# Kernel optimization log

Hardware: AMD Instinct MI355X
Metric: run time of the kernel (lower is better)

The kernel has to match this reference:

```python
import jax, jax.numpy as jnp
import numpy as np

B, H, W = 8, 448, 448
HID, EMB, OUT = 1024, 1024, 4096
P = 12544
hgrid = wgrid = H // 14  # 32


def layernorm2d(x, wgt, bias, eps=1e-6):
    # channel-wise LN over dim 1 per spatial location, as in LayerNorm2d
    u = x.mean(1, keepdims=True)
    s = ((x - u) ** 2).mean(1, keepdims=True)
    x = (x - u) / jnp.sqrt(s + eps)
    return wgt[None, :, None, None] * x + bias[None, :, None, None]


def conv2d(x, wk, b, stride):
    y = jax.lax.conv_general_dilated(x, wk, (stride, stride), 'VALID',
                                     dimension_numbers=('NCHW', 'OIHW', 'NCHW'))
    return y + b[None, :, None, None]


def grid_sample_bilinear(feat, grid):
    # feat [B,C,h,w]; grid [B,P,2] (x,y) in [-1,1]; align_corners=False, zeros padding
    Bc, C, Hh, Ww = feat.shape
    gx = (grid[..., 0] + 1.0) * 0.5 * Ww - 0.5
    gy = (grid[..., 1] + 1.0) * 0.5 * Hh - 0.5
    x0 = jnp.floor(gx); y0 = jnp.floor(gy)
    x1 = x0 + 1.0; y1 = y0 + 1.0
    wx1 = gx - x0; wx0 = 1.0 - wx1
    wy1 = gy - y0; wy0 = 1.0 - wy1
    flat = feat.reshape(Bc, C, Hh * Ww)

    def gather(ix, iy):
        valid = (ix >= 0) & (ix < Ww) & (iy >= 0) & (iy < Hh)
        ixc = jnp.clip(ix, 0, Ww - 1).astype(jnp.int32)
        iyc = jnp.clip(iy, 0, Hh - 1).astype(jnp.int32)
        idx = iyc * Ww + ixc  # [B,P]
        g = jnp.take_along_axis(flat, idx[:, None, :], axis=2)  # [B,C,P]
        return g * valid[:, None, :].astype(g.dtype)

    return (gather(x0, y0) * (wx0 * wy0)[:, None, :]
            + gather(x1, y0) * (wx1 * wy0)[:, None, :]
            + gather(x0, y1) * (wx0 * wy1)[:, None, :]
            + gather(x1, y1) * (wx1 * wy1)[:, None, :])


def forward(images, masks, image_features, point_coords, valid_mask,
            c1w, c1b, ln1w, ln1b, c2w, c2b, ln2w, ln2b, c3w, c3b, up_w, up_b):
    x = jnp.concatenate([images, masks], axis=1)  # [B,4,H,W]
    x = conv2d(x, c1w, c1b, 7)
    x = jax.nn.gelu(layernorm2d(x, ln1w, ln1b), approximate=False)
    x = conv2d(x, c2w, c2b, 2)
    x = jax.nn.gelu(layernorm2d(x, ln2w, ln2b), approximate=False)
    x = conv2d(x, c3w, c3b, 1)  # [B,EMB,h,w]
    feat = image_features.reshape(B, hgrid, wgrid, EMB).transpose(0, 3, 1, 2)
    x = x + feat
    # point_sample: coords in [0,1], mapped to [-1,1]
    sf = grid_sample_bilinear(x, 2.0 * point_coords - 1.0)  # [B,EMB,P]
    sf = sf.transpose(0, 2, 1)  # [B,P,EMB]
    vm = valid_mask.astype(sf.dtype)
    pooled = (sf * vm[:, :, None]).sum(1) / vm.sum(1)[:, None]
    pooled = jnp.nan_to_num(pooled)
    out = pooled @ up_w.T + up_b  # [B,OUT]
    return out  # single feature level: stack([out]).mean(0) == out


def setup_inputs() -> dict:
    key = jax.random.key(0)
    ks = jax.random.split(key, 12)
    rng = np.random.default_rng(0)

    masks_np = np.zeros((B, 1, H, W), np.float32)
    coords = np.full((B, P, 2), -1.0, np.float32)
    valid = np.zeros((B, P), bool)
    for b in range(B):
        y0r = int(rng.integers(0, H // 2)); x0r = int(rng.integers(0, W // 2))
        hh = int(rng.integers(H // 4, H // 2)); ww = int(rng.integers(W // 4, W // 2))
        masks_np[b, 0, y0r:y0r + hh, x0r:x0r + ww] = 1.0
        ys, xs = np.nonzero(masks_np[b, 0])
        n = len(ys)
        sel = np.sort(rng.choice(n, size=min(P, n), replace=False))
        k = len(sel)
        coords[b, :k, 0] = xs[sel] / W  # x normalized (flip of (y,x))
        coords[b, :k, 1] = ys[sel] / H  # y normalized
        valid[b, :k] = True

    s = 0.02
    return {
        'images': jax.random.normal(ks[0], (B, 3, H, W), jnp.float32),
        'masks': jnp.asarray(masks_np),
        'image_features': jax.random.normal(ks[1], (B, hgrid * wgrid, EMB), jnp.float32),
        'point_coords': jnp.asarray(coords),
        'valid_mask': jnp.asarray(valid),
        'c1w': jax.random.normal(ks[2], (HID // 4, 4, 7, 7), jnp.float32) * s,
        'c1b': jnp.zeros((HID // 4,), jnp.float32),
        'ln1w': jnp.ones((HID // 4,), jnp.float32),
        'ln1b': jnp.zeros((HID // 4,), jnp.float32),
        'c2w': jax.random.normal(ks[3], (HID, HID // 4, 2, 2), jnp.float32) * s,
        'c2b': jnp.zeros((HID,), jnp.float32),
        'ln2w': jnp.ones((HID,), jnp.float32),
        'ln2b': jnp.zeros((HID,), jnp.float32),
        'c3w': jax.random.normal(ks[4], (EMB, HID, 1, 1), jnp.float32) * s,
        'c3b': jnp.zeros((EMB,), jnp.float32),
        'up_w': jax.random.normal(ks[5], (OUT, EMB), jnp.float32) * s,
        'up_b': jnp.zeros((OUT,), jnp.float32),
    }


def reference(images, masks, image_features, point_coords, valid_mask,
              c1w, c1b, ln1w, ln1b, c2w, c2b, ln2w, ln2b, c3w, c3b, up_w, up_b):
    return forward(images, masks, image_features, point_coords, valid_mask,
                   c1w, c1b, ln1w, ln1b, c2w, c2b, ln2w, ln2b, c3w, c3b, up_w, up_b)
```

## Files before the change

kernel.cpp:

```cpp
#include <hip/hip_runtime.h>
#include <stdint.h>

#define NB 8
#define HIN 448
#define CH1 256
#define CH2 1024
#define NLOC 1024
#define M2 8192
#define M1 32768
#define K1 224
#define NPTS 12544
#define NOUT 4096
#define CAP 384
#define MC (NB * CAP)
#define M1C (MC * 4)

typedef __attribute__((ext_vector_type(8))) short bf16x8;
typedef __attribute__((ext_vector_type(4))) float f32x4;

__device__ __forceinline__ short f2bf(float f) {
  uint32_t u = __builtin_bit_cast(uint32_t, f);
  uint32_t r = (u + 0x7fffu + ((u >> 16) & 1u)) >> 16;
  return (short)r;
}
__device__ __forceinline__ float bf2f(short s) {
  return __builtin_bit_cast(float, (uint32_t)(uint16_t)s << 16);
}
__device__ __forceinline__ float gelu_f(float x) {
  return 0.5f * x * (1.0f + erff(x * 0.70710678118654752f));
}
__device__ __forceinline__ void gload_lds16(const void* g, void* l) {
  __builtin_amdgcn_global_load_lds((const __attribute__((address_space(1))) unsigned int*)g,
                                   (__attribute__((address_space(3))) unsigned int*)l, 16, 0, 0);
}

__global__ void k_prep(const float* __restrict__ c1w, const float* __restrict__ c2w,
                       short* __restrict__ c1wb, short* __restrict__ w2p,
                       float4* __restrict__ zp, int n4) {
  int i = blockIdx.x * 256 + threadIdx.x;
  if (i < n4) zp[i] = make_float4(0.f, 0.f, 0.f, 0.f);
  if (i < CH1 * K1) {
    int o = i / K1, k = i - o * K1;
    int c = k / 56, kk = k - c * 56, r = kk >> 3, cc = kk & 7;
    c1wb[i] = f2bf(cc < 7 ? c1w[((o * 4 + c) * 7 + r) * 7 + cc] : 0.0f);
  }
  if (i < CH2 * CH2) {
    int o = i >> 10, k = i & 1023;
    int pos = k >> 8, ci = k & 255;
    w2p[i] = f2bf(c2w[(size_t)(o * 256 + ci) * 4 + pos]);
  }
}

__global__ __launch_bounds__(256) void k_pts(const float* __restrict__ coords,
                                             float* __restrict__ Aw,
                                             float* __restrict__ cnt,
                                             float* __restrict__ sumAw) {
  __shared__ float lAw[NLOC];
  __shared__ int lcnt;
  __shared__ float wsum[4];
  int t = threadIdx.x;
  int b = blockIdx.x / 49;
  int blk = blockIdx.x - b * 49;
  for (int i = t; i < NLOC; i += 256) lAw[i] = 0.f;
  if (t == 0) lcnt = 0;
  __syncthreads();
  int pi = blk * 256 + t;
  float x = coords[((size_t)b * NPTS + pi) * 2];
  float y = coords[((size_t)b * NPTS + pi) * 2 + 1];
  bool valid = (x >= 0.0f);
  if (valid) {
    float gx = x * 32.0f - 0.5f, gy = y * 32.0f - 0.5f;
    float x0f = floorf(gx), y0f = floorf(gy);
    int x0 = (int)x0f, y0 = (int)y0f;
    float wx1 = gx - x0f, wx0 = 1.0f - wx1;
    float wy1 = gy - y0f, wy0 = 1.0f - wy1;
    int xs[2] = {x0, x0 + 1}, ys[2] = {y0, y0 + 1};
    float wxs[2] = {wx0, wx1}, wys[2] = {wy0, wy1};
    #pragma unroll
    for (int cy = 0; cy < 2; cy++)
      #pragma unroll
      for (int cx = 0; cx < 2; cx++) {
        int ix = xs[cx], iy = ys[cy];
        if (ix >= 0 && ix < 32 && iy >= 0 && iy < 32)
          atomicAdd(&lAw[iy * 32 + ix], wxs[cx] * wys[cy]);
      }
  }
  unsigned long long ball = __ballot(valid);
  if ((t & 63) == 0) atomicAdd(&lcnt, (int)__popcll(ball));
  __syncthreads();
  float tsum = 0.f;
  for (int i = t; i < NLOC; i += 256) {
    float v = lAw[i];
    tsum += v;
    if (v != 0.f) atomicAdd(&Aw[b * NLOC + i], v);
  }
  #pragma unroll
  for (int m = 1; m <= 32; m <<= 1) tsum += __shfl_xor(tsum, m, 64);
  if ((t & 63) == 0) wsum[t >> 6] = tsum;
  __syncthreads();
  if (t == 0) {
    float bs = wsum[0] + wsum[1] + wsum[2] + wsum[3];
    if (bs != 0.f) atomicAdd(&sumAw[b], bs);
    if (lcnt) atomicAdd(&cnt[b], (float)lcnt);
  }
}

__global__ __launch_bounds__(256) void k_compact(const float* __restrict__ Aw,
                                                 int* __restrict__ idxc,
                                                 float* __restrict__ Awc) {
  __shared__ int cnts[256], offs[256];
  int t = threadIdx.x, b = blockIdx.x;
  int base = b * 1024 + t * 4;
  float w[4];
  int c = 0;
  #pragma unroll
  for (int j = 0; j < 4; j++) { w[j] = Aw[base + j]; c += (w[j] != 0.f) ? 1 : 0; }
  cnts[t] = c;
  offs[t] = c;
  __syncthreads();
  for (int s = 1; s < 256; s <<= 1) {
    int v = (t >= s) ? offs[t - s] : 0;
    __syncthreads();
    offs[t] += v;
    __syncthreads();
  }
  int pos = b * CAP + offs[t] - cnts[t];
  int lim = (b + 1) * CAP;
  #pragma unroll
  for (int j = 0; j < 4; j++)
    if (w[j] != 0.f && pos < lim) { idxc[pos] = base + j; Awc[pos] = w[j]; pos++; }
  int total = offs[255];
  for (int i = total + t; i < CAP; i += 256) {
    idxc[b * CAP + i] = b * 1024;
    Awc[b * CAP + i] = 0.f;
  }
}

__global__ __launch_bounds__(256) void k_imc(const int* __restrict__ idxc,
                                             const float* __restrict__ images,
                                             const float* __restrict__ masks,
                                             short* __restrict__ A1c) {
  __shared__ short ct[64 * K1];
  int t = threadIdx.x;
  int i0 = blockIdx.x * 16;
  int loc = t >> 4;
  int rem = t & 15;
  int c = rem >> 2, kh = (rem >> 1) & 1, rh = rem & 1;
  int gi = idxc[i0 + loc];
  int b = gi >> 10, oy = (gi >> 5) & 31, ox = gi & 31;
  int yy = oy * 2 + kh;
  int xbase = ox * 14;
  int r0 = rh * 4, rn = rh ? 3 : 4;
  const float* plane = (c < 3)
      ? images + (size_t)(b * 3 + c) * 448 * 448
      : masks + (size_t)b * 448 * 448;
  for (int rr = 0; rr < rn; rr++) {
    int r = r0 + rr;
    const float* src = plane + (size_t)(yy * 7 + r) * 448 + xbase;
    short tmp[14];
    #pragma unroll
    for (int p = 0; p < 7; p++) {
      float2 v = *(const float2*)&src[p * 2];
      tmp[p * 2] = f2bf(v.x);
      tmp[p * 2 + 1] = f2bf(v.y);
    }
    #pragma unroll
    for (int kw = 0; kw < 2; kw++) {
      short* dst = &ct[(loc * 4 + kh * 2 + kw) * K1 + c * 56 + r * 8];
      #pragma unroll
      for (int cc = 0; cc < 7; cc++) dst[cc] = tmp[kw * 7 + cc];
      dst[7] = 0;
    }
  }
  __syncthreads();
  size_t obase = (size_t)blockIdx.x * 64 * K1;
  #pragma unroll
  for (int it = 0; it < 7; it++) {
    int p = it * 256 + t;
    *(bf16x8*)&A1c[obase + (size_t)p * 8] = *(const bf16x8*)&ct[p * 8];
  }
}

template<int KDIM, int LDC>
__global__ __launch_bounds__(256) void k_gemm64(
    const short* __restrict__ Amat, const short* __restrict__ Bmat,
    const float* __restrict__ bias, short* __restrict__ Cout) {
  __shared__ __align__(16) char Lraw[16384];
  int t = threadIdx.x, lane = t & 63, wv = t >> 6;
  int mt0 = blockIdx.x * 64;
  int nt0 = blockIdx.y * 64;
  f32x4 acc[2][2];
  #pragma unroll
  for (int i = 0; i < 2; i++)
    #pragma unroll
    for (int j = 0; j < 2; j++) acc[i][j] = (f32x4){0.f, 0.f, 0.f, 0.f};

  int srow = lane >> 2, scol = (lane & 3) * 8;
  int wm = wv >> 1, wn = wv & 1;
  int l15 = lane & 15, lg = lane >> 4;

  const short* Ap = Amat + (size_t)(mt0 + wv * 16 + srow) * KDIM;
  const short* Bp = Bmat + (size_t)(nt0 + wv * 16 + srow) * KDIM;

  auto STAGE = [&](int buf, int kt) {
    int k0 = kt * 32;
    char* As = Lraw + buf * 8192;
    char* Bs = As + 4096;
    gload_lds16(Ap + k0 + scol, As + wv * 1024);
    gload_lds16(Bp + k0 + scol, Bs + wv * 1024);
  };

  const int NT = KDIM / 32;
  STAGE(0, 0);
  __syncthreads();
  int cur = 0;
  #pragma unroll 2
  for (int kt = 0; kt < NT; kt++) {
    if (kt + 1 < NT) STAGE(cur ^ 1, kt + 1);
    const short* As = (const short*)(Lraw + cur * 8192);
    const short* Bs = As + 2048;
    bf16x8 af[2], bfr[2];
    #pragma unroll
    for (int i = 0; i < 2; i++)
      af[i] = *(const bf16x8*)&As[(wm * 32 + i * 16 + l15) * 32 + lg * 8];
    #pragma unroll
    for (int j = 0; j < 2; j++)
      bfr[j] = *(const bf16x8*)&Bs[(wn * 32 + j * 16 + l15) * 32 + lg * 8];
    #pragma unroll
    for (int i = 0; i < 2; i++)
      #pragma unroll
      for (int j = 0; j < 2; j++)
        acc[i][j] = __builtin_amdgcn_mfma_f32_16x16x32_bf16(af[i], bfr[j], acc[i][j], 0, 0, 0);
    __syncthreads();
    cur ^= 1;
  }

  short* ct = (short*)Lraw;
  #pragma unroll
  for (int i = 0; i < 2; i++)
    #pragma unroll
    for (int j = 0; j < 2; j++) {
      int cl = wn * 32 + j * 16 + l15;
      float bv = bias[nt0 + cl];
      #pragma unroll
      for (int reg = 0; reg < 4; reg++) {
        int rl = wm * 32 + i * 16 + lg * 4 + reg;
        ct[rl * 68 + cl] = f2bf(acc[i][j][reg] + bv);
      }
    }
  __syncthreads();
  #pragma unroll
  for (int it = 0; it < 2; it++) {
    int p = it * 256 + t;
    int row = p >> 3, cc = (p & 7) * 8;
    bf16x8 v = *(const bf16x8*)&ct[row * 68 + cc];
    *(bf16x8*)&Cout[(size_t)(mt0 + row) * LDC + nt0 + cc] = v;
  }
}

__global__ __launch_bounds__(256) void k_gemm2s(
    const short* __restrict__ Amat, const short* __restrict__ Bmat,
    const float* __restrict__ bias, float* __restrict__ y2p0,
    float* __restrict__ y2p1) {
  const int KDIM = 1024;
  __shared__ __align__(16) char Lraw[24576];
  int t = threadIdx.x, lane = t & 63, wv = t >> 6;
  int swz = (blockIdx.x & 7) * 96 + (blockIdx.x >> 3);
  int kz = swz / 384;
  int rem = swz - kz * 384;
  int by = rem / 24;
  int bx = rem - by * 24;
  int mt0 = bx * 128;
  int nt0 = by * 64;
  int kbase = kz * 512;
  float* outp = kz ? y2p1 : y2p0;
  f32x4 acc[4][2];
  #pragma unroll
  for (int i = 0; i < 4; i++)
    #pragma unroll
    for (int j = 0; j < 2; j++) acc[i][j] = (f32x4){0.f, 0.f, 0.f, 0.f};

  int srow = lane >> 2, scol = (lane & 3) * 8;
  int wm = wv >> 1, wn = wv & 1;
  int l15 = lane & 15, lg = lane >> 4;
  int r0 = wv * 16, r1 = 64 + wv * 16;

  auto STAGE = [&](int buf, int kt) {
    int k0 = kbase + kt * 32;
    char* As = Lraw + buf * 12288;
    char* Bs = As + 8192;
    gload_lds16(&Amat[(size_t)(mt0 + r0 + srow) * KDIM + k0 + scol], As + r0 * 64);
    gload_lds16(&Amat[(size_t)(mt0 + r1 + srow) * KDIM + k0 + scol], As + r1 * 64);
    gload_lds16(&Bmat[(size_t)(nt0 + r0 + srow) * KDIM + k0 + scol], Bs + r0 * 64);
  };

  STAGE(0, 0);
  __syncthreads();
  int cur = 0;
  #pragma unroll 2
  for (int kt = 0; kt < 16; kt++) {
    if (kt + 1 < 16) STAGE(cur ^ 1, kt + 1);
    const short* As = (const short*)(Lraw + cur * 12288);
    const short* Bs = As + 4096;
    bf16x8 af[4], bfr[2];
    #pragma unroll
    for (int i = 0; i < 4; i++)
      af[i] = *(const bf16x8*)&As[(wm * 64 + i * 16 + l15) * 32 + lg * 8];
    #pragma unroll
    for (int j = 0; j < 2; j++)
      bfr[j] = *(const bf16x8*)&Bs[(wn * 32 + j * 16 + l15) * 32 + lg * 8];
    #pragma unroll
    for (int i = 0; i < 4; i++)
      #pragma unroll
      for (int j = 0; j < 2; j++)
        acc[i][j] = __builtin_amdgcn_mfma_f32_16x16x32_bf16(af[i], bfr[j], acc[i][j], 0, 0, 0);
    __syncthreads();
    cur ^= 1;
  }

  #pragma unroll
  for (int i = 0; i < 4; i++)
    #pragma unroll
    for (int j = 0; j < 2; j++) {
      int colg = nt0 + wn * 32 + j * 16 + l15;
      float bv = kz ? 0.0f : bias[colg];
      #pragma unroll
      for (int reg = 0; reg < 4; reg++) {
        int rowg = mt0 + wm * 64 + i * 16 + lg * 4 + reg;
        outp[(size_t)rowg * 1024 + colg] = acc[i][j][reg] + bv;
      }
    }
}

__global__ __launch_bounds__(256) void k_ln1c(const short* __restrict__ y1c,
                                              const float* __restrict__ ln1w,
                                              const float* __restrict__ ln1b,
                                              short* __restrict__ act1c) {
  int t = threadIdx.x, wv = t >> 6, lane = t & 63;
  int c = lane * 4;
  float lw[4], lb[4];
  #pragma unroll
  for (int j = 0; j < 4; j++) { lw[j] = ln1w[c + j]; lb[j] = ln1b[c + j]; }
  int j0 = blockIdx.x * 64 + wv * 16;
  for (int r = 0; r < 16; r++) {
    int j = j0 + r;
    short4 v4 = *(const short4*)&y1c[(size_t)j * 256 + c];
    float xs[4] = {bf2f(v4.x), bf2f(v4.y), bf2f(v4.z), bf2f(v4.w)};
    float s = 0.f, q = 0.f;
    #pragma unroll
    for (int jj = 0; jj < 4; jj++) { s += xs[jj]; q += xs[jj] * xs[jj]; }
    #pragma unroll
    for (int mm = 1; mm <= 32; mm <<= 1) { s += __shfl_xor(s, mm, 64); q += __shfl_xor(q, mm, 64); }
    float u = s * (1.0f / 256.0f);
    float rs = rsqrtf(q * (1.0f / 256.0f) - u * u + 1e-6f);
    short o[4];
    #pragma unroll
    for (int jj = 0; jj < 4; jj++) o[jj] = f2bf(gelu_f(lw[jj] * ((xs[jj] - u) * rs) + lb[jj]));
    *(short4*)&act1c[(size_t)j * 256 + c] = make_short4(o[0], o[1], o[2], o[3]);
  }
}

__global__ __launch_bounds__(256) void k_poolboth(
    const float* __restrict__ y2p0, const float* __restrict__ y2p1,
    const float* __restrict__ feat, const int* __restrict__ idxc,
    const float* __restrict__ ln2w, const float* __restrict__ ln2b,
    const float* __restrict__ Awc, float* __restrict__ partials,
    float* __restrict__ partialsF) {
  int t = threadIdx.x, wv = t >> 6, lane = t & 63;
  int b = blockIdx.x / 12, chunk = blockIdx.x % 12;
  int base = b * CAP + chunk * 32;
  int c0 = lane * 16;
  float lw[16], lb[16], wacc[16], facc[16];
  #pragma unroll
  for (int j = 0; j < 16; j++) {
    lw[j] = ln2w[c0 + j];
    lb[j] = ln2b[c0 + j];
    wacc[j] = 0.f;
    facc[j] = 0.f;
  }
  for (int pass = 0; pass < 8; pass++) {
    int row = base + pass * 4 + wv;
    float wt = Awc[row];
    if (wt == 0.f) continue;
    const float4* fp = (const float4*)(feat + (size_t)idxc[row] * 1024 + c0);
    #pragma unroll
    for (int j = 0; j < 4; j++) {
      float4 v = fp[j];
      facc[j * 4 + 0] += wt * v.x;
      facc[j * 4 + 1] += wt * v.y;
      facc[j * 4 + 2] += wt * v.z;
      facc[j * 4 + 3] += wt * v.w;
    }
    const float4* a0 = (const float4*)(y2p0 + (size_t)row * 1024 + c0);
    const float4* a1 = (const float4*)(y2p1 + (size_t)row * 1024 + c0);
    float xs[16];
    #pragma unroll
    for (int j = 0; j < 4; j++) {
      float4 va = a0[j], vb = a1[j];
      xs[j * 4 + 0] = va.x + vb.x;
      xs[j * 4 + 1] = va.y + vb.y;
      xs[j * 4 + 2] = va.z + vb.z;
      xs[j * 4 + 3] = va.w + vb.w;
    }
    float s = 0.f, q = 0.f;
    #pragma unroll
    for (int j = 0; j < 16; j++) { s += xs[j]; q += xs[j] * xs[j]; }
    #pragma unroll
    for (int m = 1; m <= 32; m <<= 1) { s += __shfl_xor(s, m, 64); q += __shfl_xor(q, m, 64); }
    float u = s * (1.0f / 1024.0f);
    float rs = rsqrtf(q * (1.0f / 1024.0f) - u * u + 1e-6f);
    #pragma unroll
    for (int j = 0; j < 16; j++)
      wacc[j] += wt * gelu_f(lw[j] * ((xs[j] - u) * rs) + lb[j]);
  }
  float* dst = &partials[((size_t)blockIdx.x * 4 + wv) * 1024 + c0];
  float* dstF = &partialsF[((size_t)blockIdx.x * 4 + wv) * 1024 + c0];
  #pragma unroll
  for (int j = 0; j < 4; j++) {
    *(f32x4*)&dst[j * 4] = (f32x4){wacc[j * 4], wacc[j * 4 + 1], wacc[j * 4 + 2], wacc[j * 4 + 3]};
    *(f32x4*)&dstF[j * 4] = (f32x4){facc[j * 4], facc[j * 4 + 1], facc[j * 4 + 2], facc[j * 4 + 3]};
  }
}

__global__ __launch_bounds__(256) void k_red(const float* __restrict__ partials,
                                             const float* __restrict__ partialsF,
                                             float* __restrict__ pa,
                                             float* __restrict__ pf) {
  int c = blockIdx.x * 256 + threadIdx.x;
  int b = c >> 10, ch = c & 1023;
  const float* p = partials + (size_t)(b * 48) * 1024 + ch;
  const float* pF = partialsF + (size_t)(b * 48) * 1024 + ch;
  float s = 0.f, sf = 0.f;
  #pragma unroll 8
  for (int j = 0; j < 48; j++) {
    s += p[(size_t)j * 1024];
    sf += pF[(size_t)j * 1024];
  }
  pa[c] = s;
  pf[c] = sf;
}

__global__ __launch_bounds__(256) void k_mix(const float* __restrict__ pa,
                                             const float* __restrict__ pf,
                                             const float* __restrict__ sumAw,
                                             const float* __restrict__ cnt,
                                             const float* __restrict__ c3w,
                                             const float* __restrict__ c3b,
                                             float* __restrict__ zn) {
  __shared__ float pl[8192];
  int t = threadIdx.x;
  for (int idx = t; idx < 2048; idx += 256)
    ((float4*)pl)[idx] = ((const float4*)pa)[idx];
  __syncthreads();
  int wv = t >> 6, lane = t & 63;
  int c = blockIdx.x * 4 + wv;
  float w[16];
  #pragma unroll
  for (int i = 0; i < 16; i++) w[i] = c3w[(size_t)c * 1024 + i * 64 + lane];
  float s[8];
  #pragma unroll
  for (int b = 0; b < 8; b++) s[b] = 0.f;
  #pragma unroll
  for (int i = 0; i < 16; i++) {
    int k = i * 64 + lane;
    #pragma unroll
    for (int b = 0; b < 8; b++) s[b] += w[i] * pl[b * 1024 + k];
  }
  #pragma unroll
  for (int m = 1; m <= 32; m <<= 1)
    #pragma unroll
    for (int b = 0; b < 8; b++) s[b] += __shfl_xor(s[b], m, 64);
  if (lane < 8) {
    float cv = cnt[lane];
    float z = s[lane] + sumAw[lane] * c3b[c] + pf[lane * 1024 + c];
    zn[lane * 1024 + c] = cv > 0.f ? z / cv : 0.f;
  }
}

__global__ __launch_bounds__(256) void k_out(const float* __restrict__ zn,
                                             const float* __restrict__ up_w,
                                             const float* __restrict__ up_b,
                                             float* __restrict__ out) {
  __shared__ float pl[8192];
  int t = threadIdx.x;
  for (int idx = t; idx < 2048; idx += 256)
    ((float4*)pl)[idx] = ((const float4*)zn)[idx];
  __syncthreads();
  int wv = t >> 6, lane = t & 63;
  int o = blockIdx.x * 4 + wv;
  float w[16];
  #pragma unroll
  for (int i = 0; i < 16; i++) w[i] = up_w[(size_t)o * 1024 + i * 64 + lane];
  float s[8];
  #pragma unroll
  for (int b = 0; b < 8; b++) s[b] = 0.f;
  #pragma unroll
  for (int i = 0; i < 16; i++) {
    int k = i * 64 + lane;
    #pragma unroll
    for (int b = 0; b < 8; b++) s[b] += w[i] * pl[b * 1024 + k];
  }
  #pragma unroll
  for (int m = 1; m <= 32; m <<= 1)
    #pragma unroll
    for (int b = 0; b < 8; b++) s[b] += __shfl_xor(s[b], m, 64);
  if (lane < 8) out[(size_t)lane * NOUT + o] = s[lane] + up_b[o];
}

extern "C" void kernel_launch(void* const* d_in, const int* in_sizes, int n_in,
                              void* d_out, int out_size, void* d_ws, size_t ws_size,
                              hipStream_t stream) {
  const float* images = (const float*)d_in[0];
  const float* masks  = (const float*)d_in[1];
  const float* feat   = (const float*)d_in[2];
  const float* coords = (const float*)d_in[3];
  const float* c1w  = (const float*)d_in[5];
  const float* c1b  = (const float*)d_in[6];
  const float* ln1w = (const float*)d_in[7];
  const float* ln1b = (const float*)d_in[8];
  const float* c2w  = (const float*)d_in[9];
  const float* c2b  = (const float*)d_in[10];
  const float* ln2w = (const float*)d_in[11];
  const float* ln2b = (const float*)d_in[12];
  const float* c3w  = (const float*)d_in[13];
  const float* c3b  = (const float*)d_in[14];
  const float* up_w = (const float*)d_in[15];
  const float* up_b = (const float*)d_in[16];
  float* out = (float*)d_out;

  char* ws = (char*)d_ws;
  size_t off = 0;
  auto alloc = [&](size_t bytes) -> void* {
    void* p = ws + off;
    off = (off + bytes + 255) & ~(size_t)255;
    return p;
  };
  float* Aw    = (float*)alloc(8192 * 4);
  float* cnt   = (float*)alloc(8 * 4);
  float* sumAw = (float*)alloc(8 * 4);
  size_t zeroBytes = off;
  int*   idxc  = (int*)alloc(MC * 4);
  float* Awc   = (float*)alloc(MC * 4);
  float* pa    = (float*)alloc(8192 * 4);
  float* pf    = (float*)alloc(8192 * 4);
  float* partials  = (float*)alloc((size_t)384 * 1024 * 4);
  float* partialsF = (float*)alloc((size_t)384 * 1024 * 4);
  float* zn   = (float*)alloc(8192 * 4);
  short* c1wb = (short*)alloc((size_t)CH1 * K1 * 2);
  short* w2p  = (short*)alloc((size_t)CH2 * CH2 * 2);
  short* A1c  = (short*)alloc((size_t)M1C * K1 * 2);
  short* y1c  = (short*)alloc((size_t)M1C * 256 * 2);
  short* act1c = (short*)alloc((size_t)MC * 1024 * 2);
  float* y2p0 = (float*)alloc((size_t)MC * 1024 * 4);
  float* y2p1 = (float*)alloc((size_t)MC * 1024 * 4);

  int n4 = (int)(zeroBytes / 16);
  k_prep<<<4096, 256, 0, stream>>>(c1w, c2w, c1wb, w2p, (float4*)d_ws, n4);
  k_pts<<<NB * 49, 256, 0, stream>>>(coords, Aw, cnt, sumAw);
  k_compact<<<NB, 256, 0, stream>>>(Aw, idxc, Awc);
  k_imc<<<MC / 16, 256, 0, stream>>>(idxc, images, masks, A1c);
  k_gemm64<K1, 256><<<dim3(M1C / 64, 4), 256, 0, stream>>>(A1c, c1wb, c1b, y1c);
  k_ln1c<<<M1C / 64, 256, 0, stream>>>(y1c, ln1w, ln1b, act1c);
  k_gemm2s<<<768, 256, 0, stream>>>(act1c, w2p, c2b, y2p0, y2p1);
  k_poolboth<<<96, 256, 0, stream>>>(y2p0, y2p1, feat, idxc, ln2w, ln2b, Awc, partials, partialsF);
  k_red<<<32, 256, 0, stream>>>(partials, partialsF, pa, pf);
  k_mix<<<256, 256, 0, stream>>>(pa, pf, sumAw, cnt, c3w, c3b, zn);
  k_out<<<NOUT / 4, 256, 0, stream>>>(zn, up_w, up_b, out);
}
```

Before: 110.3 us.

## Split pooling across more blocks and reduce partials with LDS plus atomics

```diff
diff --git a/kernel.cpp b/kernel.cpp
--- a/kernel.cpp
+++ b/kernel.cpp
@@ -364,11 +364,13 @@
     const float* __restrict__ y2p0, const float* __restrict__ y2p1,
     const float* __restrict__ feat, const int* __restrict__ idxc,
     const float* __restrict__ ln2w, const float* __restrict__ ln2b,
-    const float* __restrict__ Awc, float* __restrict__ partials,
-    float* __restrict__ partialsF) {
+    const float* __restrict__ Awc, float* __restrict__ pa,
+    float* __restrict__ pf) {
+  __shared__ float lsA[4][1024];
+  __shared__ float lsF[4][1024];
   int t = threadIdx.x, wv = t >> 6, lane = t & 63;
-  int b = blockIdx.x / 12, chunk = blockIdx.x % 12;
-  int base = b * CAP + chunk * 32;
+  int b = blockIdx.x / 48, chunk = blockIdx.x % 48;
+  int base = b * CAP + chunk * 8;
   int c0 = lane * 16;
   float lw[16], lb[16], wacc[16], facc[16];
   #pragma unroll
@@ -378,7 +380,8 @@
     wacc[j] = 0.f;
     facc[j] = 0.f;
   }
-  for (int pass = 0; pass < 8; pass++) {
+  #pragma unroll
+  for (int pass = 0; pass < 2; pass++) {
     int row = base + pass * 4 + wv;
     float wt = Awc[row];
     if (wt == 0.f) continue;
@@ -413,31 +416,21 @@
     for (int j = 0; j < 16; j++)
       wacc[j] += wt * gelu_f(lw[j] * ((xs[j] - u) * rs) + lb[j]);
   }
-  float* dst = &partials[((size_t)blockIdx.x * 4 + wv) * 1024 + c0];
-  float* dstF = &partialsF[((size_t)blockIdx.x * 4 + wv) * 1024 + c0];
   #pragma unroll
   for (int j = 0; j < 4; j++) {
-    *(f32x4*)&dst[j * 4] = (f32x4){wacc[j * 4], wacc[j * 4 + 1], wacc[j * 4 + 2], wacc[j * 4 + 3]};
-    *(f32x4*)&dstF[j * 4] = (f32x4){facc[j * 4], facc[j * 4 + 1], facc[j * 4 + 2], facc[j * 4 + 3]};
-  }
-}
-
-__global__ __launch_bounds__(256) void k_red(const float* __restrict__ partials,
-                                             const float* __restrict__ partialsF,
-                                             float* __restrict__ pa,
-                                             float* __restrict__ pf) {
-  int c = blockIdx.x * 256 + threadIdx.x;
-  int b = c >> 10, ch = c & 1023;
-  const float* p = partials + (size_t)(b * 48) * 1024 + ch;
-  const float* pF = partialsF + (size_t)(b * 48) * 1024 + ch;
-  float s = 0.f, sf = 0.f;
-  #pragma unroll 8
-  for (int j = 0; j < 48; j++) {
-    s += p[(size_t)j * 1024];
-    sf += pF[(size_t)j * 1024];
-  }
-  pa[c] = s;
-  pf[c] = sf;
+    *(f32x4*)&lsA[wv][c0 + j * 4] = (f32x4){wacc[j * 4], wacc[j * 4 + 1], wacc[j * 4 + 2], wacc[j * 4 + 3]};
+    *(f32x4*)&lsF[wv][c0 + j * 4] = (f32x4){facc[j * 4], facc[j * 4 + 1], facc[j * 4 + 2], facc[j * 4 + 3]};
+  }
+  __syncthreads();
+  int cb = t * 4;
+  #pragma unroll
+  for (int j = 0; j < 4; j++) {
+    int c = cb + j;
+    float sa = lsA[0][c] + lsA[1][c] + lsA[2][c] + lsA[3][c];
+    float sf = lsF[0][c] + lsF[1][c] + lsF[2][c] + lsF[3][c];
+    if (sa != 0.f) atomicAdd(&pa[b * 1024 + c], sa);
+    if (sf != 0.f) atomicAdd(&pf[b * 1024 + c], sf);
+  }
 }
 
 __global__ __launch_bounds__(256) void k_mix(const float* __restrict__ pa,
@@ -538,13 +531,11 @@
   float* Aw    = (float*)alloc(8192 * 4);
   float* cnt   = (float*)alloc(8 * 4);
   float* sumAw = (float*)alloc(8 * 4);
+  float* pa    = (float*)alloc(8192 * 4);
+  float* pf    = (float*)alloc(8192 * 4);
   size_t zeroBytes = off;
   int*   idxc  = (int*)alloc(MC * 4);
   float* Awc   = (float*)alloc(MC * 4);
-  float* pa    = (float*)alloc(8192 * 4);
-  float* pf    = (float*)alloc(8192 * 4);
-  float* partials  = (float*)alloc((size_t)384 * 1024 * 4);
-  float* partialsF = (float*)alloc((size_t)384 * 1024 * 4);
   float* zn   = (float*)alloc(8192 * 4);
   short* c1wb = (short*)alloc((size_t)CH1 * K1 * 2);
   short* w2p  = (short*)alloc((size_t)CH2 * CH2 * 2);
@@ -562,8 +553,7 @@
   k_gemm64<K1, 256><<<dim3(M1C / 64, 4), 256, 0, stream>>>(A1c, c1wb, c1b, y1c);
   k_ln1c<<<M1C / 64, 256, 0, stream>>>(y1c, ln1w, ln1b, act1c);
   k_gemm2s<<<768, 256, 0, stream>>>(act1c, w2p, c2b, y2p0, y2p1);
-  k_poolboth<<<96, 256, 0, stream>>>(y2p0, y2p1, feat, idxc, ln2w, ln2b, Awc, partials, partialsF);
-  k_red<<<32, 256, 0, stream>>>(partials, partialsF, pa, pf);
+  k_poolboth<<<384, 256, 0, stream>>>(y2p0, y2p1, feat, idxc, ln2w, ln2b, Awc, pa, pf);
   k_mix<<<256, 256, 0, stream>>>(pa, pf, sumAw, cnt, c3w, c3b, zn);
   k_out<<<NOUT / 4, 256, 0, stream>>>(zn, up_w, up_b, out);
 }
```

Measured after the change: 96.04 us (median of 2 runs). 12.9% less time.
